# Optimization experiments

Hardware: AMD Instinct MI355X
Metric: run time of the kernel (lower is better)

The kernel has to match this reference:

```python
import jax, jax.numpy as jnp
import numpy as np

B, S, D, H = 2, 2048, 1024, 16
HD = D // H  # head size = 64

def setup_inputs() -> dict:
    key = jax.random.key(0)
    ks = jax.random.split(key, 12)
    sc = 0.02
    return {
        "hidden_states": jax.random.normal(ks[0], (B, S, D), jnp.float32),
        "attention_mask": jnp.zeros((B, S), jnp.float32),  # additive mask (0 = attend)
        "position_bias": jax.random.normal(ks[1], (H, S, S), jnp.float32) * sc,
        "Wq": jax.random.normal(ks[2], (D, D), jnp.float32) * sc,
        "bq": jnp.zeros((D,), jnp.float32),
        "Wk": jax.random.normal(ks[3], (D, D), jnp.float32) * sc,
        "bk": jnp.zeros((D,), jnp.float32),
        "Wv": jax.random.normal(ks[4], (D, D), jnp.float32) * sc,
        "bv": jnp.zeros((D,), jnp.float32),
        "Wo": jax.random.normal(ks[5], (D, D), jnp.float32) * sc,
        "bo": jnp.zeros((D,), jnp.float32),
    }

def reference(hidden_states, attention_mask, position_bias, Wq, bq, Wk, bk, Wv, bv, Wo, bo):
    b, s, _ = hidden_states.shape
    def heads(x):
        # [B,S,D] -> [B,H,S,HD]
        return x.reshape(b, s, H, HD).transpose(0, 2, 1, 3)
    q = heads(hidden_states @ Wq + bq)
    k = heads(hidden_states @ Wk + bk)
    v = heads(hidden_states @ Wv + bv)
    scores = jnp.einsum("bhqd,bhkd->bhqk", q, k) / jnp.sqrt(jnp.float32(HD))
    scores = scores + position_bias[None]                 # [1,H,S,S]
    scores = scores + attention_mask[:, None, None, :]    # [B,1,1,S]
    probs = jax.nn.softmax(scores, axis=-1)
    # dropout is identity in eval mode
    ctx = jnp.einsum("bhqk,bhkd->bhqd", probs, v)
    ctx = ctx.transpose(0, 2, 1, 3).reshape(b, s, D)
    return ctx @ Wo + bo
```

## Files before the change

### kernel.cpp

```cpp
#include <hip/hip_runtime.h>
#include <hip/hip_bf16.h>

#define B_  2
#define S_  2048
#define D_  1024
#define H_  16
#define HD_ 64
#define M_  (B_ * S_)

typedef unsigned short u16;
typedef __attribute__((ext_vector_type(8))) short short8;
typedef __attribute__((ext_vector_type(4))) float f32x4;

#define MFMA16(a, b, c) __builtin_amdgcn_mfma_f32_16x16x32_bf16(a, b, c, 0, 0, 0)

__device__ __forceinline__ u16 f2bf(float f) {
    union { float f; unsigned u; } v; v.f = f;
    unsigned r = v.u + 0x7FFFu + ((v.u >> 16) & 1u);
    return (u16)(r >> 16);
}

__device__ __forceinline__ void gl_lds16(const void* g, void* lds) {
    __builtin_amdgcn_global_load_lds(
        (const __attribute__((address_space(1))) unsigned int*)g,
        (__attribute__((address_space(3))) unsigned int*)lds, 16, 0, 0);
}

__global__ __launch_bounds__(256) void cvt_bf16(const float* __restrict__ x,
                                                u16* __restrict__ y) {
    const int i = (blockIdx.x * 256 + threadIdx.x) * 4;
    const float4 v = *(const float4*)(x + i);
    ushort4 o;
    o.x = f2bf(v.x); o.y = f2bf(v.y); o.z = f2bf(v.z); o.w = f2bf(v.w);
    *(ushort4*)(y + i) = o;
}

__global__ __launch_bounds__(256) void wt_trans(
    const float* __restrict__ w0, const float* __restrict__ w1,
    const float* __restrict__ w2, const float* __restrict__ w3,
    u16* __restrict__ t0, u16* __restrict__ t1,
    u16* __restrict__ t2, u16* __restrict__ t3) {
    const float* W; u16* T;
    switch (blockIdx.z) {
        case 0: W = w0; T = t0; break;
        case 1: W = w1; T = t1; break;
        case 2: W = w2; T = t2; break;
        default: W = w3; T = t3; break;
    }
    __shared__ float t[32][33];
    const int tid = threadIdx.x;
    const int kt = blockIdx.x, nt = blockIdx.y;
    const int r = tid >> 3, c4 = (tid & 7) * 4;
    const float4 v = *(const float4*)&W[(size_t)(kt * 32 + r) * D_ + nt * 32 + c4];
    t[c4 + 0][r] = v.x; t[c4 + 1][r] = v.y; t[c4 + 2][r] = v.z; t[c4 + 3][r] = v.w;
    __syncthreads();
    ushort4 o;
    o.x = f2bf(t[r][c4 + 0]); o.y = f2bf(t[r][c4 + 1]);
    o.z = f2bf(t[r][c4 + 2]); o.w = f2bf(t[r][c4 + 3]);
    *(ushort4*)&T[(size_t)(nt * 32 + r) * D_ + kt * 32 + c4] = o;
}

__global__ __launch_bounds__(256) void v_trans(const u16* __restrict__ V,
                                               u16* __restrict__ VT) {
    __shared__ u16 t[64][72];
    const int bh = blockIdx.x, s0 = blockIdx.y * 64;
    const int tid = threadIdx.x;
    const int ss = tid >> 2, cq = tid & 3;
    const u16* src = V + ((size_t)bh * S_ + s0 + ss) * HD_ + cq * 16;
    u16 buf[16];
    *(uint4*)&buf[0] = *(const uint4*)&src[0];
    *(uint4*)&buf[8] = *(const uint4*)&src[8];
#pragma unroll
    for (int j = 0; j < 16; ++j) t[cq * 16 + j][ss] = buf[j];
    __syncthreads();
    const int dd = tid >> 2;
    u16 ob[16];
#pragma unroll
    for (int j = 0; j < 16; ++j) ob[j] = t[dd][cq * 16 + j];
    u16* dst = VT + ((size_t)bh * HD_ + dd) * S_ + s0 + cq * 16;
    *(uint4*)&dst[0] = *(uint4*)&ob[0];
    *(uint4*)&dst[8] = *(uint4*)&ob[8];
}

__global__ __launch_bounds__(256, 3) void gemm_bt_bf16(
    const u16* __restrict__ A, const u16* __restrict__ Bt,
    const float* __restrict__ bi0, const float* __restrict__ bi1, const float* __restrict__ bi2,
    void* __restrict__ o0, void* __restrict__ o1, void* __restrict__ o2,
    int mode) {
    __shared__ __align__(16) char smem[32768];

    const int tid = threadIdx.x;
    const int wave = tid >> 6, lane = tid & 63;
    const int quad = lane >> 4, l15 = lane & 15;
    const int wm = wave >> 1, wn = wave & 1;
    const int bm = blockIdx.x * 128, bn = blockIdx.y * 128;

    const int sel = bn >> 10;
    const float* bias = (sel == 0) ? bi0 : (sel == 1) ? bi1 : bi2;
    void* outp = (sel == 0) ? o0 : (sel == 1) ? o1 : o2;

    f32x4 acc[4][4];
#pragma unroll
    for (int i = 0; i < 4; ++i)
#pragma unroll
        for (int j = 0; j < 4; ++j) acc[i][j] = (f32x4)0.f;

    const int c0 = wave * 128 + lane;
#pragma unroll
    for (int i = 0; i < 2; ++i) {
        const int c = c0 + i * 64;
        const int row = c >> 2, e = c & 3;
        gl_lds16(A  + (size_t)(bm + row) * D_ + e * 8,
                 smem + (wave * 2 + i) * 1024);
        gl_lds16(Bt + (size_t)(bn + row) * D_ + e * 8,
                 smem + 16384 + (wave * 2 + i) * 1024);
    }
    __syncthreads();

    for (int it = 0; it < 32; ++it) {
        const int cur = it & 1;
        if (it < 31) {
            const int k0n = (it + 1) * 32;
            const int nb = cur ^ 1;
#pragma unroll
            for (int i = 0; i < 2; ++i) {
                const int c = c0 + i * 64;
                const int row = c >> 2, e = c & 3;
                gl_lds16(A  + (size_t)(bm + row) * D_ + k0n + e * 8,
                         smem + nb * 8192 + (wave * 2 + i) * 1024);
                gl_lds16(Bt + (size_t)(bn + row) * D_ + k0n + e * 8,
                         smem + 16384 + nb * 8192 + (wave * 2 + i) * 1024);
            }
        }

        short8 aF[4], bF[4];
#pragma unroll
        for (int mt = 0; mt < 4; ++mt)
            aF[mt] = *(const short8*)(smem + cur * 8192 +
                     ((wm * 64 + mt * 16 + l15) * 32 + quad * 8) * 2);
#pragma unroll
        for (int nt = 0; nt < 4; ++nt)
            bF[nt] = *(const short8*)(smem + 16384 + cur * 8192 +
                     ((wn * 64 + nt * 16 + l15) * 32 + quad * 8) * 2);
#pragma unroll
        for (int mt = 0; mt < 4; ++mt)
#pragma unroll
            for (int nt = 0; nt < 4; ++nt)
                acc[mt][nt] = MFMA16(aF[mt], bF[nt], acc[mt][nt]);

        __syncthreads();
    }

    float bv[4];
#pragma unroll
    for (int nt = 0; nt < 4; ++nt)
        bv[nt] = bias[(bn & 1023) + wn * 64 + nt * 16 + l15];

    if (mode == 1) {
        u16* ob = (u16*)outp;
#pragma unroll
        for (int mt = 0; mt < 4; ++mt)
#pragma unroll
            for (int nt = 0; nt < 4; ++nt)
#pragma unroll
                for (int r = 0; r < 4; ++r) {
                    const int m = bm + wm * 64 + mt * 16 + quad * 4 + r;
                    const int n = (bn & 1023) + wn * 64 + nt * 16 + l15;
                    const int bb = m >> 11, ss = m & (S_ - 1);
                    const int hh = n >> 6,  dd = n & (HD_ - 1);
                    ob[(((size_t)bb * H_ + hh) * S_ + ss) * HD_ + dd] =
                        f2bf(acc[mt][nt][r] + bv[nt]);
                }
    } else {
        float* of = (float*)outp;
#pragma unroll
        for (int mt = 0; mt < 4; ++mt)
#pragma unroll
            for (int nt = 0; nt < 4; ++nt)
#pragma unroll
                for (int r = 0; r < 4; ++r) {
                    const int m = bm + wm * 64 + mt * 16 + quad * 4 + r;
                    const int n = bn + wn * 64 + nt * 16 + l15;
                    of[(size_t)m * D_ + n] = acc[mt][nt][r] + bv[nt];
                }
    }
}

#define AQP_OFF 0
#define AK_OFF  8192
#define AV_OFF  24576

__global__ __launch_bounds__(256, 4) void attn_mfma(
    const u16* __restrict__ Qg, const u16* __restrict__ Kg, const u16* __restrict__ VTg,
    const float* __restrict__ pb, const float* __restrict__ mask,
    u16* __restrict__ Cb) {
    __shared__ __align__(16) char smem[40960];
    u16* PsU = (u16*)(smem + AQP_OFF);

    const int tid = threadIdx.x;
    const int wave = tid >> 6, lane = tid & 63;
    const int quad = lane >> 4, l15 = lane & 15;

    const int b = blockIdx.x & 1, qblk = blockIdx.x >> 1;
    const int h = blockIdx.y;
    const int q0 = qblk * 64;

    const size_t bh = (size_t)b * H_ + h;
    const u16* Qb  = Qg  + bh * (S_ * HD_);
    const u16* Kb  = Kg  + bh * (S_ * HD_);
    const u16* VTb = VTg + bh * (HD_ * S_);

#pragma unroll
    for (int i = 0; i < 2; ++i) {
        const int c = (wave * 2 + i) * 64 + lane;
        const int row = c >> 3, e = c & 7, dc = e ^ (row & 7);
        gl_lds16(Qb + (size_t)(q0 + row) * HD_ + dc * 8,
                 smem + AQP_OFF + (wave * 2 + i) * 1024);
        gl_lds16(Kb + (size_t)row * HD_ + dc * 8,
                 smem + AK_OFF + (wave * 2 + i) * 1024);
        gl_lds16(VTb + (size_t)row * S_ + dc * 8,
                 smem + AV_OFF + (wave * 2 + i) * 1024);
    }
    __syncthreads();

    short8 aQ[2];
#pragma unroll
    for (int kc = 0; kc < 2; ++kc) {
        const int q = wave * 16 + l15;
        const int dc = kc * 4 + quad;
        aQ[kc] = *(const short8*)(smem + AQP_OFF + (q * 8 + (dc ^ (q & 7))) * 16);
    }

    u16* Pw = PsU + (l15 >> 3) * 512 + (wave * 16 + quad * 4) * 8 + (l15 & 7);

    f32x4 O[4];
    float lst[4];
#pragma unroll
    for (int nt = 0; nt < 4; ++nt) O[nt] = (f32x4)0.f;
#pragma unroll
    for (int r = 0; r < 4; ++r) lst[r] = 0.f;

    for (int kt = 0; kt < S_ / 64; ++kt) {
        const int k0 = kt * 64;
        const int cur = kt & 1;

        if (kt < S_ / 64 - 1) {
            const int nb = cur ^ 1;
            const int k0n = k0 + 64;
#pragma unroll
            for (int i = 0; i < 2; ++i) {
                const int c = (wave * 2 + i) * 64 + lane;
                const int row = c >> 3, e = c & 7, dc = e ^ (row & 7);
                gl_lds16(Kb + (size_t)(k0n + row) * HD_ + dc * 8,
                         smem + AK_OFF + nb * 8192 + (wave * 2 + i) * 1024);
                gl_lds16(VTb + (size_t)row * S_ + k0n + dc * 8,
                         smem + AV_OFF + nb * 8192 + (wave * 2 + i) * 1024);
            }
        }

        float mk[4], pbv[4][4];
#pragma unroll
        for (int nt = 0; nt < 4; ++nt) mk[nt] = mask[b * S_ + k0 + nt * 16 + l15];
#pragma unroll
        for (int r = 0; r < 4; ++r) {
            const int qg = q0 + wave * 16 + quad * 4 + r;
            const float* rowp = pb + ((size_t)h * S_ + qg) * S_ + k0;
#pragma unroll
            for (int nt = 0; nt < 4; ++nt) pbv[r][nt] = rowp[nt * 16 + l15];
        }

        f32x4 sc[4];
#pragma unroll
        for (int nt = 0; nt < 4; ++nt) sc[nt] = (f32x4)0.f;
#pragma unroll
        for (int nt = 0; nt < 4; ++nt)
#pragma unroll
            for (int kc = 0; kc < 2; ++kc) {
                const int kk = nt * 16 + l15;
                const int dc = kc * 4 + quad;
                const short8 bK = *(const short8*)(smem + AK_OFF + cur * 8192 +
                                   (kk * 8 + (dc ^ (kk & 7))) * 16);
                sc[nt] = MFMA16(aQ[kc], bK, sc[nt]);
            }

#pragma unroll
        for (int r = 0; r < 4; ++r) {
            const float s0 = fmaf(sc[0][r], 0.125f, pbv[r][0] + mk[0]);
            const float s1 = fmaf(sc[1][r], 0.125f, pbv[r][1] + mk[1]);
            const float s2 = fmaf(sc[2][r], 0.125f, pbv[r][2] + mk[2]);
            const float s3 = fmaf(sc[3][r], 0.125f, pbv[r][3] + mk[3]);
            const float p0 = __expf(s0), p1 = __expf(s1);
            const float p2 = __expf(s2), p3 = __expf(s3);
            lst[r] += (p0 + p1) + (p2 + p3);
            Pw[0 * 1024 + r * 8] = f2bf(p0);
            Pw[1 * 1024 + r * 8] = f2bf(p1);
            Pw[2 * 1024 + r * 8] = f2bf(p2);
            Pw[3 * 1024 + r * 8] = f2bf(p3);
        }

        short8 aP[2];
#pragma unroll
        for (int kc = 0; kc < 2; ++kc)
            aP[kc] = *(const short8*)(PsU + (kc * 4 + quad) * 512 + (wave * 16 + l15) * 8);
#pragma unroll
        for (int nt = 0; nt < 4; ++nt)
#pragma unroll
            for (int kc = 0; kc < 2; ++kc) {
                const int d = nt * 16 + l15;
                const int dc = kc * 4 + quad;
                const short8 bV = *(const short8*)(smem + AV_OFF + cur * 8192 +
                                   (d * 8 + (dc ^ (d & 7))) * 16);
                O[nt] = MFMA16(aP[kc], bV, O[nt]);
            }

        __syncthreads();
    }

#pragma unroll
    for (int r = 0; r < 4; ++r) {
#pragma unroll
        for (int off = 1; off < 16; off <<= 1)
            lst[r] += __shfl_xor(lst[r], off, 64);
        const float inv = 1.f / lst[r];
        const int s = q0 + wave * 16 + quad * 4 + r;
        u16* dst = Cb + ((size_t)b * S_ + s) * D_ + h * HD_;
#pragma unroll
        for (int nt = 0; nt < 4; ++nt)
            dst[nt * 16 + l15] = f2bf(O[nt][r] * inv);
    }
}

extern "C" void kernel_launch(void* const* d_in, const int* in_sizes, int n_in,
                              void* d_out, int out_size, void* d_ws, size_t ws_size,
                              hipStream_t stream) {
    const float* X    = (const float*)d_in[0];
    const float* mask = (const float*)d_in[1];
    const float* pb   = (const float*)d_in[2];
    const float* Wq   = (const float*)d_in[3];
    const float* bq   = (const float*)d_in[4];
    const float* Wk   = (const float*)d_in[5];
    const float* bk   = (const float*)d_in[6];
    const float* Wv   = (const float*)d_in[7];
    const float* bv   = (const float*)d_in[8];
    const float* Wo   = (const float*)d_in[9];
    const float* bo   = (const float*)d_in[10];
    float* out = (float*)d_out;

    u16* Xb    = (u16*)d_ws;
    u16* WtQKV = Xb    + (size_t)M_ * D_;
    u16* Wto   = WtQKV + (size_t)3 * D_ * D_;
    u16* Qw    = Wto   + (size_t)D_ * D_;
    u16* Kw    = Qw    + (size_t)M_ * D_;
    u16* Vw    = Kw    + (size_t)M_ * D_;
    u16* Cb    = Vw    + (size_t)M_ * D_;
    u16* VTw   = Cb    + (size_t)M_ * D_;

    cvt_bf16<<<(M_ * D_) / (256 * 4), 256, 0, stream>>>(X, Xb);
    wt_trans<<<dim3(32, 32, 4), 256, 0, stream>>>(
        Wq, Wk, Wv, Wo, WtQKV, WtQKV + (size_t)D_ * D_, WtQKV + (size_t)2 * D_ * D_, Wto);

    gemm_bt_bf16<<<dim3(M_ / 128, 3 * D_ / 128), 256, 0, stream>>>(
        Xb, WtQKV, bq, bk, bv, Qw, Kw, Vw, 1);

    v_trans<<<dim3(B_ * H_, S_ / 64), 256, 0, stream>>>(Vw, VTw);

    attn_mfma<<<dim3((S_ / 64) * B_, H_), 256, 0, stream>>>(Qw, Kw, VTw, pb, mask, Cb);

    gemm_bt_bf16<<<dim3(M_ / 128, D_ / 128), 256, 0, stream>>>(
        Cb, Wto, bo, bo, bo, out, out, out, 0);
}
```

Baseline: 508.2 us.

## Fuse prep kernels, write V transposed from GEMM, load attention operands from global

Merges the X conversion and weight transposes into one prep launch. The QKV GEMM epilogue now writes V directly in transposed [B,H,HD,S] layout, which removes the separate v_trans kernel and its workspace. The attention kernel drops LDS staging and double buffering for K and V and reads MFMA operands straight from global memory, keeping only a per-wave P buffer in LDS and no block barriers. This removes launches, a transpose pass and synchronisation, but each wave now issues redundant, less coalesced global loads for K and V.

Measured after the change: 628.1 us. +23.6%, slower.

```diff
diff --git a/kernel.cpp b/kernel.cpp
--- a/kernel.cpp
+++ b/kernel.cpp
@@ -26,60 +26,42 @@
         (__attribute__((address_space(3))) unsigned int*)lds, 16, 0, 0);
 }
 
-__global__ __launch_bounds__(256) void cvt_bf16(const float* __restrict__ x,
-                                                u16* __restrict__ y) {
-    const int i = (blockIdx.x * 256 + threadIdx.x) * 4;
-    const float4 v = *(const float4*)(x + i);
-    ushort4 o;
-    o.x = f2bf(v.x); o.y = f2bf(v.y); o.z = f2bf(v.z); o.w = f2bf(v.w);
-    *(ushort4*)(y + i) = o;
-}
-
-__global__ __launch_bounds__(256) void wt_trans(
+__global__ __launch_bounds__(256) void prep(
+    const float* __restrict__ X,
     const float* __restrict__ w0, const float* __restrict__ w1,
     const float* __restrict__ w2, const float* __restrict__ w3,
+    u16* __restrict__ Xb,
     u16* __restrict__ t0, u16* __restrict__ t1,
     u16* __restrict__ t2, u16* __restrict__ t3) {
-    const float* W; u16* T;
-    switch (blockIdx.z) {
-        case 0: W = w0; T = t0; break;
-        case 1: W = w1; T = t1; break;
-        case 2: W = w2; T = t2; break;
-        default: W = w3; T = t3; break;
-    }
-    __shared__ float t[32][33];
+    const int z = blockIdx.z;
     const int tid = threadIdx.x;
-    const int kt = blockIdx.x, nt = blockIdx.y;
     const int r = tid >> 3, c4 = (tid & 7) * 4;
-    const float4 v = *(const float4*)&W[(size_t)(kt * 32 + r) * D_ + nt * 32 + c4];
-    t[c4 + 0][r] = v.x; t[c4 + 1][r] = v.y; t[c4 + 2][r] = v.z; t[c4 + 3][r] = v.w;
-    __syncthreads();
-    ushort4 o;
-    o.x = f2bf(t[r][c4 + 0]); o.y = f2bf(t[r][c4 + 1]);
-    o.z = f2bf(t[r][c4 + 2]); o.w = f2bf(t[r][c4 + 3]);
-    *(ushort4*)&T[(size_t)(nt * 32 + r) * D_ + kt * 32 + c4] = o;
-}
-
-__global__ __launch_bounds__(256) void v_trans(const u16* __restrict__ V,
-                                               u16* __restrict__ VT) {
-    __shared__ u16 t[64][72];
-    const int bh = blockIdx.x, s0 = blockIdx.y * 64;
-    const int tid = threadIdx.x;
-    const int ss = tid >> 2, cq = tid & 3;
-    const u16* src = V + ((size_t)bh * S_ + s0 + ss) * HD_ + cq * 16;
-    u16 buf[16];
-    *(uint4*)&buf[0] = *(const uint4*)&src[0];
-    *(uint4*)&buf[8] = *(const uint4*)&src[8];
-#pragma unroll
-    for (int j = 0; j < 16; ++j) t[cq * 16 + j][ss] = buf[j];
-    __syncthreads();
-    const int dd = tid >> 2;
-    u16 ob[16];
-#pragma unroll
-    for (int j = 0; j < 16; ++j) ob[j] = t[dd][cq * 16 + j];
-    u16* dst = VT + ((size_t)bh * HD_ + dd) * S_ + s0 + cq * 16;
-    *(uint4*)&dst[0] = *(uint4*)&ob[0];
-    *(uint4*)&dst[8] = *(uint4*)&ob[8];
+
+    if (z < 4) {
+        const float* W; u16* T;
+        switch (z) {
+            case 0: W = w0; T = t0; break;
+            case 1: W = w1; T = t1; break;
+            case 2: W = w2; T = t2; break;
+            default: W = w3; T = t3; break;
+        }
+        __shared__ float t[32][33];
+        const int kt = blockIdx.x, nt = blockIdx.y;
+        const float4 v = *(const float4*)&W[(size_t)(kt * 32 + r) * D_ + nt * 32 + c4];
+        t[c4 + 0][r] = v.x; t[c4 + 1][r] = v.y; t[c4 + 2][r] = v.z; t[c4 + 3][r] = v.w;
+        __syncthreads();
+        ushort4 o;
+        o.x = f2bf(t[r][c4 + 0]); o.y = f2bf(t[r][c4 + 1]);
+        o.z = f2bf(t[r][c4 + 2]); o.w = f2bf(t[r][c4 + 3]);
+        *(ushort4*)&T[(size_t)(nt * 32 + r) * D_ + kt * 32 + c4] = o;
+    } else {
+        const size_t off = (size_t)(z - 4) * 1024 * 1024;
+        const int row = blockIdx.x * 32 + r, col = blockIdx.y * 32 + c4;
+        const float4 v = *(const float4*)&X[off + (size_t)row * 1024 + col];
+        ushort4 o;
+        o.x = f2bf(v.x); o.y = f2bf(v.y); o.z = f2bf(v.z); o.w = f2bf(v.w);
+        *(ushort4*)&Xb[off + (size_t)row * 1024 + col] = o;
+    }
 }
 
 __global__ __launch_bounds__(256, 3) void gemm_bt_bf16(
@@ -158,19 +140,38 @@
 
     if (mode == 1) {
         u16* ob = (u16*)outp;
-#pragma unroll
-        for (int mt = 0; mt < 4; ++mt)
-#pragma unroll
-            for (int nt = 0; nt < 4; ++nt)
-#pragma unroll
-                for (int r = 0; r < 4; ++r) {
-                    const int m = bm + wm * 64 + mt * 16 + quad * 4 + r;
+        if (sel < 2) {
+#pragma unroll
+            for (int mt = 0; mt < 4; ++mt)
+#pragma unroll
+                for (int nt = 0; nt < 4; ++nt)
+#pragma unroll
+                    for (int r = 0; r < 4; ++r) {
+                        const int m = bm + wm * 64 + mt * 16 + quad * 4 + r;
+                        const int n = (bn & 1023) + wn * 64 + nt * 16 + l15;
+                        const int bb = m >> 11, ss = m & (S_ - 1);
+                        const int hh = n >> 6,  dd = n & (HD_ - 1);
+                        ob[(((size_t)bb * H_ + hh) * S_ + ss) * HD_ + dd] =
+                            f2bf(acc[mt][nt][r] + bv[nt]);
+                    }
+        } else {
+#pragma unroll
+            for (int mt = 0; mt < 4; ++mt) {
+                const int m0 = bm + wm * 64 + mt * 16 + quad * 4;
+                const int bb = m0 >> 11, ss = m0 & (S_ - 1);
+#pragma unroll
+                for (int nt = 0; nt < 4; ++nt) {
                     const int n = (bn & 1023) + wn * 64 + nt * 16 + l15;
-                    const int bb = m >> 11, ss = m & (S_ - 1);
-                    const int hh = n >> 6,  dd = n & (HD_ - 1);
-                    ob[(((size_t)bb * H_ + hh) * S_ + ss) * HD_ + dd] =
-                        f2bf(acc[mt][nt][r] + bv[nt]);
+                    const int hh = n >> 6, dd = n & (HD_ - 1);
+                    ushort4 w;
+                    w.x = f2bf(acc[mt][nt][0] + bv[nt]);
+                    w.y = f2bf(acc[mt][nt][1] + bv[nt]);
+                    w.z = f2bf(acc[mt][nt][2] + bv[nt]);
+                    w.w = f2bf(acc[mt][nt][3] + bv[nt]);
+                    *(ushort4*)&ob[(((size_t)bb * H_ + hh) * HD_ + dd) * S_ + ss] = w;
                 }
+            }
+        }
     } else {
         float* of = (float*)outp;
 #pragma unroll
@@ -186,16 +187,11 @@
     }
 }
 
-#define AQP_OFF 0
-#define AK_OFF  8192
-#define AV_OFF  24576
-
 __global__ __launch_bounds__(256, 4) void attn_mfma(
     const u16* __restrict__ Qg, const u16* __restrict__ Kg, const u16* __restrict__ VTg,
     const float* __restrict__ pb, const float* __restrict__ mask,
     u16* __restrict__ Cb) {
-    __shared__ __align__(16) char smem[40960];
-    u16* PsU = (u16*)(smem + AQP_OFF);
+    __shared__ __align__(16) u16 Ps[4 * 1024];
 
     const int tid = threadIdx.x;
     const int wave = tid >> 6, lane = tid & 63;
@@ -204,34 +200,20 @@
     const int b = blockIdx.x & 1, qblk = blockIdx.x >> 1;
     const int h = blockIdx.y;
     const int q0 = qblk * 64;
+    const int qw = q0 + wave * 16;
 
     const size_t bh = (size_t)b * H_ + h;
     const u16* Qb  = Qg  + bh * (S_ * HD_);
     const u16* Kb  = Kg  + bh * (S_ * HD_);
     const u16* VTb = VTg + bh * (HD_ * S_);
 
-#pragma unroll
-    for (int i = 0; i < 2; ++i) {
-        const int c = (wave * 2 + i) * 64 + lane;
-        const int row = c >> 3, e = c & 7, dc = e ^ (row & 7);
-        gl_lds16(Qb + (size_t)(q0 + row) * HD_ + dc * 8,
-                 smem + AQP_OFF + (wave * 2 + i) * 1024);
-        gl_lds16(Kb + (size_t)row * HD_ + dc * 8,
-                 smem + AK_OFF + (wave * 2 + i) * 1024);
-        gl_lds16(VTb + (size_t)row * S_ + dc * 8,
-                 smem + AV_OFF + (wave * 2 + i) * 1024);
-    }
-    __syncthreads();
-
     short8 aQ[2];
 #pragma unroll
-    for (int kc = 0; kc < 2; ++kc) {
-        const int q = wave * 16 + l15;
-        const int dc = kc * 4 + quad;
-        aQ[kc] = *(const short8*)(smem + AQP_OFF + (q * 8 + (dc ^ (q & 7))) * 16);
-    }
-
-    u16* Pw = PsU + (l15 >> 3) * 512 + (wave * 16 + quad * 4) * 8 + (l15 & 7);
+    for (int kc = 0; kc < 2; ++kc)
+        aQ[kc] = *(const short8*)&Qb[(size_t)(qw + l15) * HD_ + kc * 32 + quad * 8];
+
+    u16* Pw = Ps + wave * 1024 + (l15 >> 3) * 128 + quad * 32 + (l15 & 7);
+    const u16* Pr = Ps + wave * 1024 + quad * 128 + l15 * 8;
 
     f32x4 O[4];
     float lst[4];
@@ -242,46 +224,31 @@
 
     for (int kt = 0; kt < S_ / 64; ++kt) {
         const int k0 = kt * 64;
-        const int cur = kt & 1;
-
-        if (kt < S_ / 64 - 1) {
-            const int nb = cur ^ 1;
-            const int k0n = k0 + 64;
-#pragma unroll
-            for (int i = 0; i < 2; ++i) {
-                const int c = (wave * 2 + i) * 64 + lane;
-                const int row = c >> 3, e = c & 7, dc = e ^ (row & 7);
-                gl_lds16(Kb + (size_t)(k0n + row) * HD_ + dc * 8,
-                         smem + AK_OFF + nb * 8192 + (wave * 2 + i) * 1024);
-                gl_lds16(VTb + (size_t)row * S_ + k0n + dc * 8,
-                         smem + AV_OFF + nb * 8192 + (wave * 2 + i) * 1024);
-            }
-        }
+
+        short8 bK[4][2];
+#pragma unroll
+        for (int nt = 0; nt < 4; ++nt)
+#pragma unroll
+            for (int kc = 0; kc < 2; ++kc)
+                bK[nt][kc] = *(const short8*)
+                    &Kb[(size_t)(k0 + nt * 16 + l15) * HD_ + kc * 32 + quad * 8];
 
         float mk[4], pbv[4][4];
 #pragma unroll
         for (int nt = 0; nt < 4; ++nt) mk[nt] = mask[b * S_ + k0 + nt * 16 + l15];
 #pragma unroll
         for (int r = 0; r < 4; ++r) {
-            const int qg = q0 + wave * 16 + quad * 4 + r;
-            const float* rowp = pb + ((size_t)h * S_ + qg) * S_ + k0;
+            const float* rowp = pb + ((size_t)h * S_ + (qw + quad * 4 + r)) * S_ + k0;
 #pragma unroll
             for (int nt = 0; nt < 4; ++nt) pbv[r][nt] = rowp[nt * 16 + l15];
         }
 
         f32x4 sc[4];
 #pragma unroll
-        for (int nt = 0; nt < 4; ++nt) sc[nt] = (f32x4)0.f;
-#pragma unroll
-        for (int nt = 0; nt < 4; ++nt)
-#pragma unroll
-            for (int kc = 0; kc < 2; ++kc) {
-                const int kk = nt * 16 + l15;
-                const int dc = kc * 4 + quad;
-                const short8 bK = *(const short8*)(smem + AK_OFF + cur * 8192 +
-                                   (kk * 8 + (dc ^ (kk & 7))) * 16);
-                sc[nt] = MFMA16(aQ[kc], bK, sc[nt]);
-            }
+        for (int nt = 0; nt < 4; ++nt) {
+            sc[nt] = MFMA16(aQ[0], bK[nt][0], (f32x4)0.f);
+            sc[nt] = MFMA16(aQ[1], bK[nt][1], sc[nt]);
+        }
 
 #pragma unroll
         for (int r = 0; r < 4; ++r) {
@@ -292,28 +259,24 @@
             const float p0 = __expf(s0), p1 = __expf(s1);
             const float p2 = __expf(s2), p3 = __expf(s3);
             lst[r] += (p0 + p1) + (p2 + p3);
-            Pw[0 * 1024 + r * 8] = f2bf(p0);
-            Pw[1 * 1024 + r * 8] = f2bf(p1);
-            Pw[2 * 1024 + r * 8] = f2bf(p2);
-            Pw[3 * 1024 + r * 8] = f2bf(p3);
+            Pw[0 * 256 + r * 8] = f2bf(p0);
+            Pw[1 * 256 + r * 8] = f2bf(p1);
+            Pw[2 * 256 + r * 8] = f2bf(p2);
+            Pw[3 * 256 + r * 8] = f2bf(p3);
         }
 
         short8 aP[2];
 #pragma unroll
         for (int kc = 0; kc < 2; ++kc)
-            aP[kc] = *(const short8*)(PsU + (kc * 4 + quad) * 512 + (wave * 16 + l15) * 8);
+            aP[kc] = *(const short8*)(Pr + kc * 512);
 #pragma unroll
         for (int nt = 0; nt < 4; ++nt)
 #pragma unroll
             for (int kc = 0; kc < 2; ++kc) {
-                const int d = nt * 16 + l15;
-                const int dc = kc * 4 + quad;
-                const short8 bV = *(const short8*)(smem + AV_OFF + cur * 8192 +
-                                   (d * 8 + (dc ^ (d & 7))) * 16);
+                const short8 bV = *(const short8*)
+                    &VTb[(size_t)(nt * 16 + l15) * S_ + k0 + kc * 32 + quad * 8];
                 O[nt] = MFMA16(aP[kc], bV, O[nt]);
             }
-
-        __syncthreads();
     }
 
 #pragma unroll
@@ -322,7 +285,7 @@
         for (int off = 1; off < 16; off <<= 1)
             lst[r] += __shfl_xor(lst[r], off, 64);
         const float inv = 1.f / lst[r];
-        const int s = q0 + wave * 16 + quad * 4 + r;
+        const int s = qw + quad * 4 + r;
         u16* dst = Cb + ((size_t)b * S_ + s) * D_ + h * HD_;
 #pragma unroll
         for (int nt = 0; nt < 4; ++nt)
@@ -351,18 +314,15 @@
     u16* Wto   = WtQKV + (size_t)3 * D_ * D_;
     u16* Qw    = Wto   + (size_t)D_ * D_;
     u16* Kw    = Qw    + (size_t)M_ * D_;
-    u16* Vw    = Kw    + (size_t)M_ * D_;
-    u16* Cb    = Vw    + (size_t)M_ * D_;
-    u16* VTw   = Cb    + (size_t)M_ * D_;
-
-    cvt_bf16<<<(M_ * D_) / (256 * 4), 256, 0, stream>>>(X, Xb);
-    wt_trans<<<dim3(32, 32, 4), 256, 0, stream>>>(
-        Wq, Wk, Wv, Wo, WtQKV, WtQKV + (size_t)D_ * D_, WtQKV + (size_t)2 * D_ * D_, Wto);
+    u16* VTw   = Kw    + (size_t)M_ * D_;
+    u16* Cb    = VTw   + (size_t)M_ * D_;
+
+    prep<<<dim3(32, 32, 8), 256, 0, stream>>>(
+        X, Wq, Wk, Wv, Wo, Xb,
+        WtQKV, WtQKV + (size_t)D_ * D_, WtQKV + (size_t)2 * D_ * D_, Wto);
 
     gemm_bt_bf16<<<dim3(M_ / 128, 3 * D_ / 128), 256, 0, stream>>>(
-        Xb, WtQKV, bq, bk, bv, Qw, Kw, Vw, 1);
-
-    v_trans<<<dim3(B_ * H_, S_ / 64), 256, 0, stream>>>(Vw, VTw);
+        Xb, WtQKV, bq, bk, bv, Qw, Kw, VTw, 1);
 
     attn_mfma<<<dim3((S_ / 64) * B_, H_), 256, 0, stream>>>(Qw, Kw, VTw, pb, mask, Cb);
 
```
